# Optimization experiments

Measured on AMD Instinct MI355X. Metric: run time of the kernel, lower is better.

Reference implementation:

```python
import jax, jax.numpy as jnp
import numpy as np

B, T, D, H, V = 512, 40, 300, 200, 50257  # batch, max_length, embed_size, lstm_dimension, vocab
FORGET_BIAS = 1.0  # TF1 LSTMCell default


def setup_inputs() -> dict:
    key = jax.random.key(0)
    ks = jax.random.split(key, 8)
    s = 0.02
    return {
        "input_ids": jax.random.randint(ks[0], (B, T), 0, V, dtype=jnp.int32),
        "lengths": jax.random.randint(ks[1], (B,), 1, T + 1, dtype=jnp.int32),
        "emb": (jax.random.normal(ks[2], (V, D)) * s).astype(jnp.float32),
        "Wx": (jax.random.normal(ks[3], (D, 4 * H)) * s).astype(jnp.float32),
        "Wh": (jax.random.normal(ks[4], (H, 4 * H)) * s).astype(jnp.float32),
        "b": jnp.zeros((4 * H,), jnp.float32),
        "U": (jax.random.normal(ks[5], (H, D)) * s).astype(jnp.float32),
        "b1": jnp.zeros((D,), jnp.float32),
        "b2": jnp.zeros((V,), jnp.float32),
    }


def lstm_last_cell(x, lengths, Wx, Wh, b):
    """TF1 LSTMCell (gate order i, j, f, o; forget_bias=1) unrolled like
    dynamic_rnn with sequence_length: state frozen past each row's length.
    Returns final cell state c of shape [B, H]."""
    Bq = x.shape[0]
    Hq = Wh.shape[0]
    xt = jnp.transpose(x, (1, 0, 2))                      # [T, B, D]
    xproj = xt @ Wx + b                                    # [T, B, 4H] precomputed input GEMM
    tmask = (jnp.arange(x.shape[1])[:, None] < lengths[None, :])[..., None]  # [T, B, 1]

    def step(carry, inp):
        c, h = carry
        xp, m = inp
        gates = xp + h @ Wh                                # [B, 4H]
        i, j, f, o = jnp.split(gates, 4, axis=-1)
        c_new = jax.nn.sigmoid(f + FORGET_BIAS) * c + jax.nn.sigmoid(i) * jnp.tanh(j)
        h_new = jax.nn.sigmoid(o) * jnp.tanh(c_new)
        c = jnp.where(m, c_new, c)
        h = jnp.where(m, h_new, h)
        return (c, h), None

    init = (jnp.zeros((Bq, Hq), x.dtype), jnp.zeros((Bq, Hq), x.dtype))
    (c, _h), _ = jax.lax.scan(step, init, (xproj, tmask))
    return c


def reference(input_ids, lengths, emb, Wx, Wh, b, U, b1, b2):
    x = emb[input_ids]                                     # [B, T, D] embedding lookup
    c = lstm_last_cell(x, lengths, Wx, Wh, b)              # [B, H] final cell state (state.c)
    h1 = jax.nn.relu(c @ U + b1)                           # [B, D]
    # dropout with keep_prob=1 at eval -> identity
    return h1 @ emb.T + b2                                 # [B, V] tied-weight logits
```

## Files before the change

### kernel.cpp

```cpp
#include <hip/hip_runtime.h>
#include <stdint.h>

#define TT_  40
#define GP_  896
#define HKP_ 224
#define V_   50257
#define VP_  50432

typedef __attribute__((ext_vector_type(4))) float f32x4;
typedef __attribute__((ext_vector_type(8))) short s16x8;

__device__ __forceinline__ ushort bfrn(float f) {
  union { float f; uint32_t u; } x; x.f = f;
  return (ushort)((x.u + 0x7fffu + ((x.u >> 16) & 1u)) >> 16);
}
__device__ __forceinline__ float bl16(uint32_t u) { return __uint_as_float(u << 16); }
__device__ __forceinline__ float bh16(uint32_t u) { return __uint_as_float(u & 0xffff0000u); }
__device__ __forceinline__ float sigm(float x) { return 1.f / (1.f + __expf(-x)); }
__device__ __forceinline__ float tanh_f(float x) { return 1.f - 2.f / (__expf(2.f*x) + 1.f); }

template<int N> struct IC { static constexpr int v = N; };

__global__ void k_prep_emb(const float* __restrict__ emb, ushort* __restrict__ emb_bf) {
  const int idx = blockIdx.x * 256 + threadIdx.x;
  const int v = idx / 80, kc = idx % 80;
  ushort4 o = {0, 0, 0, 0};
  if (v < V_ && kc < 75) {
    const float4 f = *(const float4*)(emb + (size_t)v * 300 + kc * 4);
    o.x = bfrn(f.x); o.y = bfrn(f.y); o.z = bfrn(f.z); o.w = bfrn(f.w);
  }
  *(ushort4*)(emb_bf + (size_t)v * 320 + kc * 4) = o;
}

__global__ void k_prep_small(const float* __restrict__ Wx, const float* __restrict__ Wh,
                             const float* __restrict__ U, ushort* __restrict__ Wxp,
                             ushort* __restrict__ Whp, float* __restrict__ Ut) {
  int idx = blockIdx.x * 256 + threadIdx.x;
  if (idx < 896 * 320) {
    const int colp = idx / 320, k = idx % 320;
    const int n = colp >> 2, g = colp & 3;
    const float v = (colp < 800 && k < 300) ? Wx[(size_t)k * 800 + g * 200 + n] : 0.f;
    Wxp[idx] = bfrn(v);
    return;
  }
  idx -= 896 * 320;
  if (idx < 896 * 224) {
    const int colp = idx / 224, k = idx % 224;
    const int n = colp >> 2, g = colp & 3;
    const float v = (colp < 800 && k < 200) ? Wh[(size_t)k * 800 + g * 200 + n] : 0.f;
    Whp[idx] = bfrn(v);
    return;
  }
  idx -= 896 * 224;
  if (idx < 300 * 200) {
    const int d = idx / 200, h = idx % 200;
    Ut[idx] = U[(size_t)h * 300 + d];
  }
}

__global__ __launch_bounds__(256) void k_xproj(
    const int* __restrict__ ids, const ushort* __restrict__ emb_bf,
    const ushort* __restrict__ Wxp, const float* __restrict__ bias,
    ushort* __restrict__ xp) {
  __shared__ ushort bsm[70 * 512];
  const int tid = threadIdx.x;
  const int w = tid >> 6, lane = tid & 63;
  const int l15 = lane & 15, q = lane >> 4;
  const int wgm = blockIdx.x, wgn = blockIdx.y;
  const int t = wgm >> 3;
  const int bbase = (wgm & 7) << 6;
  const int n0 = wgn * 112;

  for (int s = w; s < 70; s += 4) {
    const int tl = s / 10, kb = s % 10;
    const s16x8 v = *(const s16x8*)(Wxp + (size_t)(n0 + tl * 16 + l15) * 320 + kb * 32 + q * 8);
    *(s16x8*)(&bsm[s * 512 + lane * 8]) = v;
  }
  const int brow = bbase + w * 16 + l15;
  const int id = ids[brow * TT_ + t];
  const ushort* arow = emb_bf + (size_t)id * 320;
  __syncthreads();

  f32x4 acc[7];
  const f32x4 z = {0.f, 0.f, 0.f, 0.f};
#pragma unroll
  for (int tl = 0; tl < 7; ++tl) acc[tl] = z;
  for (int kb = 0; kb < 10; ++kb) {
    const s16x8 af = *(const s16x8*)(arow + kb * 32 + q * 8);
#pragma unroll
    for (int tl = 0; tl < 7; ++tl) {
      const s16x8 bfv = *(const s16x8*)(&bsm[(tl * 10 + kb) * 512 + lane * 8]);
      acc[tl] = __builtin_amdgcn_mfma_f32_16x16x32_bf16(af, bfv, acc[tl], 0, 0, 0);
    }
  }
  const int rowbase = t * 512 + bbase + w * 16 + q * 4;
#pragma unroll
  for (int tl = 0; tl < 7; ++tl) {
    const int colp = n0 + tl * 16 + l15;
    const float bv = (colp < 800) ? bias[(colp & 3) * 200 + (colp >> 2)] : 0.f;
#pragma unroll
    for (int r = 0; r < 4; ++r)
      xp[(size_t)(rowbase + r) * GP_ + colp] = bfrn(acc[tl][r] + bv);
  }
}

__global__ __launch_bounds__(512) __attribute__((amdgpu_waves_per_eu(2, 2)))
void k_lstm(
    const ushort* __restrict__ xp, const ushort* __restrict__ Whp,
    const int* __restrict__ lengths, const float* __restrict__ Ut,
    const float* __restrict__ b1v, ushort* __restrict__ h1bf) {
  __shared__ ushort h_lds[2][3584];
  __shared__ ushort wh56_lds[57344];
  __shared__ float  c_lds[16 * 228];

  const int tid = threadIdx.x;
  const int w = tid >> 6, lane = tid & 63;
  const int l15 = lane & 15, q = lane >> 4;
  const int b0 = blockIdx.x << 4;
  const int len = lengths[b0 + l15];

  s16x8 whf[7][5];
#pragma unroll
  for (int tl = 0; tl < 7; ++tl) {
    const ushort* wr = Whp + (size_t)((w * 7 + tl) * 16 + l15) * HKP_;
#pragma unroll
    for (int kb = 0; kb < 5; ++kb)
      whf[tl][kb] = *(const s16x8*)(wr + kb * 32 + q * 8);
    *(s16x8*)(&wh56_lds[(w * 7 + tl) * 1024 + lane * 8])       = *(const s16x8*)(wr + 160 + q * 8);
    *(s16x8*)(&wh56_lds[(w * 7 + tl) * 1024 + 512 + lane * 8]) = *(const s16x8*)(wr + 192 + q * 8);
  }
  for (int i = tid; i < 3584; i += 512) ((uint32_t*)h_lds)[i] = 0;
  for (int i = tid; i < 16 * 228; i += 512) c_lds[i] = 0.f;

  int hwoff[7];
  unsigned nokm = 0;
#pragma unroll
  for (int tl = 0; tl < 7; ++tl) {
    const int T0 = w * 7 + tl;
    const int n = T0 * 4 + q;
    if (n < 200) nokm |= (1u << tl);
    hwoff[tl] = (n >> 5) * 1024 + (l15 + (((n >> 3) & 3) << 4)) * 16 + (n & 7) * 2;
  }
  const int cidx = l15 * 228 + w * 28 + q;
  const char* xbase = (const char*)xp + (size_t)(b0 + l15) * (GP_ * 2) + w * 224 + q * 8;

  __syncthreads();

  auto step = [&](int t, auto BUFC) {
    constexpr int BUF = decltype(BUFC)::v;
    const char* xpp = xbase + (size_t)t * (512 * GP_ * 2);
    uint2 xv[7];
#pragma unroll
    for (int tl = 0; tl < 7; ++tl) xv[tl] = *(const uint2*)(xpp + tl * 32);

    f32x4 acc[7];
    const f32x4 z = {0.f, 0.f, 0.f, 0.f};
#pragma unroll
    for (int tl = 0; tl < 7; ++tl) acc[tl] = z;
#pragma unroll
    for (int kb = 0; kb < 7; ++kb) {
      const s16x8 hh = *(const s16x8*)(&h_lds[BUF][kb * 512 + lane * 8]);
#pragma unroll
      for (int tl = 0; tl < 7; ++tl) {
        s16x8 a;
        if (kb < 5) a = whf[tl][kb];
        else        a = *(const s16x8*)(&wh56_lds[(w * 7 + tl) * 1024 + (kb - 5) * 512 + lane * 8]);
        acc[tl] = __builtin_amdgcn_mfma_f32_16x16x32_bf16(a, hh, acc[tl], 0, 0, 0);
      }
    }
    const bool act = (t < len);
#pragma unroll
    for (int tl = 0; tl < 7; ++tl) {
      const float g0 = acc[tl][0] + bl16(xv[tl].x);
      const float g1 = acc[tl][1] + bh16(xv[tl].x);
      const float g2 = acc[tl][2] + bl16(xv[tl].y);
      const float g3 = acc[tl][3] + bh16(xv[tl].y);
      const bool nok = (nokm >> tl) & 1;
      ushort hv = *(const ushort*)((const char*)(&h_lds[BUF][0]) + hwoff[tl]);
      if (act && nok) {
        const float cold = c_lds[cidx + 4 * tl];
        const float sf = sigm(g2 + 1.f);
        const float si = sigm(g0);
        const float tj = tanh_f(g1);
        const float cn = sf * cold + si * tj;
        c_lds[cidx + 4 * tl] = cn;
        hv = bfrn(sigm(g3) * tanh_f(cn));
      }
      if (nok)
        *(ushort*)((char*)(&h_lds[BUF ^ 1][0]) + hwoff[tl]) = hv;
    }
    __syncthreads();
  };

  for (int tt = 0; tt < TT_ / 2; ++tt) {
    step(2 * tt,     IC<0>{});
    step(2 * tt + 1, IC<1>{});
  }

  for (int i = tid; i < 4800; i += 512) {
    const int col = i >> 4, row = i & 15;
    const float* ut = Ut + col * 200;
    const float* cr = &c_lds[row * 228];
    float s = 0.f;
    for (int k = 0; k < 200; k += 4) {
      const float4 cc = *(const float4*)(cr + k);
      const float4 uu = *(const float4*)(ut + k);
      s += cc.x * uu.x + cc.y * uu.y + cc.z * uu.z + cc.w * uu.w;
    }
    s += b1v[col];
    h1bf[(size_t)(b0 + row) * 320 + col] = bfrn(fmaxf(s, 0.f));
  }
  if (tid < 320) {
    const int row = tid & 15, col = 300 + (tid >> 4);
    h1bf[(size_t)(b0 + row) * 320 + col] = 0;
  }
}

__global__ __launch_bounds__(256) void k_out(
    const ushort* __restrict__ h1bf, const ushort* __restrict__ emb_bf,
    const float* __restrict__ b2, float* __restrict__ out) {
  const int tid = threadIdx.x;
  const int w = tid >> 6, lane = tid & 63;
  const int l15 = lane & 15, q = lane >> 4;
  const int m0 = blockIdx.y << 6;
  const int n0 = blockIdx.x * 256 + w * 64;
  f32x4 acc[4][4];
  const f32x4 z = {0.f, 0.f, 0.f, 0.f};
#pragma unroll
  for (int a = 0; a < 4; ++a)
#pragma unroll
    for (int b = 0; b < 4; ++b) acc[a][b] = z;
  for (int kb = 0; kb < 10; ++kb) {
    s16x8 af[4], bfv[4];
#pragma unroll
    for (int mt = 0; mt < 4; ++mt)
      af[mt] = *(const s16x8*)(h1bf + (size_t)(m0 + mt * 16 + l15) * 320 + kb * 32 + q * 8);
#pragma unroll
    for (int nt = 0; nt < 4; ++nt)
      bfv[nt] = *(const s16x8*)(emb_bf + (size_t)(n0 + nt * 16 + l15) * 320 + kb * 32 + q * 8);
#pragma unroll
    for (int mt = 0; mt < 4; ++mt)
#pragma unroll
      for (int nt = 0; nt < 4; ++nt)
        acc[mt][nt] = __builtin_amdgcn_mfma_f32_16x16x32_bf16(af[mt], bfv[nt], acc[mt][nt], 0, 0, 0);
  }
#pragma unroll
  for (int nt = 0; nt < 4; ++nt) {
    const int col = n0 + nt * 16 + l15;
    if (col < V_) {
      const float bb = b2[col];
#pragma unroll
      for (int mt = 0; mt < 4; ++mt) {
        const int row = m0 + mt * 16 + q * 4;
#pragma unroll
        for (int r = 0; r < 4; ++r)
          out[(size_t)(row + r) * V_ + col] = acc[mt][nt][r] + bb;
      }
    }
  }
}

extern "C" void kernel_launch(void* const* d_in, const int* in_sizes, int n_in,
                              void* d_out, int out_size, void* d_ws, size_t ws_size,
                              hipStream_t stream) {
  (void)in_sizes; (void)n_in; (void)out_size; (void)ws_size;
  const int*   ids  = (const int*)d_in[0];
  const int*   lens = (const int*)d_in[1];
  const float* emb  = (const float*)d_in[2];
  const float* Wx   = (const float*)d_in[3];
  const float* Wh   = (const float*)d_in[4];
  const float* bg   = (const float*)d_in[5];
  const float* U    = (const float*)d_in[6];
  const float* b1   = (const float*)d_in[7];
  const float* b2   = (const float*)d_in[8];
  float* out = (float*)d_out;

  char* ws = (char*)d_ws;
  ushort* emb_bf = (ushort*)(ws);
  ushort* Wxp    = (ushort*)(ws + 32276480);
  ushort* Whp    = (ushort*)(ws + 32849920);
  float*  Ut     = (float*)(ws + 33251328);
  ushort* h1bf   = (ushort*)(ws + 33491328);
  ushort* xp     = (ushort*)((char*)d_out + 66226176);

  k_prep_emb  <<<15760, 256, 0, stream>>>(emb, emb_bf);
  k_prep_small<<<2139,  256, 0, stream>>>(Wx, Wh, U, Wxp, Whp, Ut);
  k_xproj     <<<dim3(320, 8), 256, 0, stream>>>(ids, emb_bf, Wxp, bg, xp);
  k_lstm      <<<32, 512, 0, stream>>>(xp, Whp, lens, Ut, b1, h1bf);
  k_out       <<<dim3(197, 8), 256, 0, stream>>>(h1bf, emb_bf, b2, out);
}
```

Before: 388.4 us.

## Spread LSTM recurrence over 14 waves and store xproj in MFMA fragment order

The LSTM block grows from 8 to 16 waves, with 14 active ones each owning 4 gate tiles instead of 7. This shortens the serial per-step MFMA chain and the gate math on the critical path. The xproj kernel now writes its output in a tiled layout that matches each wave's fragment, so the per-step loads in the recurrence are contiguous and coalesced. The cost is more waves per CU contending at each step's barrier, and the waves_per_eu hint is dropped, which may change register allocation.

```diff
diff --git a/kernel.cpp b/kernel.cpp
--- a/kernel.cpp
+++ b/kernel.cpp
@@ -2,7 +2,6 @@
 #include <stdint.h>
 
 #define TT_  40
-#define GP_  896
 #define HKP_ 224
 #define V_   50257
 #define VP_  50432
@@ -93,18 +92,21 @@
       acc[tl] = __builtin_amdgcn_mfma_f32_16x16x32_bf16(af, bfv, acc[tl], 0, 0, 0);
     }
   }
-  const int rowbase = t * 512 + bbase + w * 16 + q * 4;
+  const int g16 = ((wgm & 7) << 2) + w;
+  ushort* xpb = xp + ((size_t)t * 32 + g16) * 14336;
 #pragma unroll
   for (int tl = 0; tl < 7; ++tl) {
     const int colp = n0 + tl * 16 + l15;
+    const int T0 = colp >> 4;
     const float bv = (colp < 800) ? bias[(colp & 3) * 200 + (colp >> 2)] : 0.f;
+    const int base = T0 * 256 + (l15 >> 2) * 64 + (l15 & 3);
 #pragma unroll
     for (int r = 0; r < 4; ++r)
-      xp[(size_t)(rowbase + r) * GP_ + colp] = bfrn(acc[tl][r] + bv);
-  }
-}
-
-__global__ __launch_bounds__(512) __attribute__((amdgpu_waves_per_eu(2, 2)))
+      xpb[base + (q * 4 + r) * 4] = bfrn(acc[tl][r] + bv);
+  }
+}
+
+__global__ __launch_bounds__(1024)
 void k_lstm(
     const ushort* __restrict__ xp, const ushort* __restrict__ Whp,
     const int* __restrict__ lengths, const float* __restrict__ Ut,
@@ -116,78 +118,84 @@
   const int tid = threadIdx.x;
   const int w = tid >> 6, lane = tid & 63;
   const int l15 = lane & 15, q = lane >> 4;
-  const int b0 = blockIdx.x << 4;
+  const int g16 = blockIdx.x;
+  const int b0 = g16 << 4;
   const int len = lengths[b0 + l15];
-
-  s16x8 whf[7][5];
-#pragma unroll
-  for (int tl = 0; tl < 7; ++tl) {
-    const ushort* wr = Whp + (size_t)((w * 7 + tl) * 16 + l15) * HKP_;
-#pragma unroll
-    for (int kb = 0; kb < 5; ++kb)
-      whf[tl][kb] = *(const s16x8*)(wr + kb * 32 + q * 8);
-    *(s16x8*)(&wh56_lds[(w * 7 + tl) * 1024 + lane * 8])       = *(const s16x8*)(wr + 160 + q * 8);
-    *(s16x8*)(&wh56_lds[(w * 7 + tl) * 1024 + 512 + lane * 8]) = *(const s16x8*)(wr + 192 + q * 8);
-  }
-  for (int i = tid; i < 3584; i += 512) ((uint32_t*)h_lds)[i] = 0;
-  for (int i = tid; i < 16 * 228; i += 512) c_lds[i] = 0.f;
-
-  int hwoff[7];
+  const bool work = (w < 14);
+
+  s16x8 whf[4][5];
+  if (work) {
+#pragma unroll
+    for (int tl = 0; tl < 4; ++tl) {
+      const int T0 = w * 4 + tl;
+      const ushort* wr = Whp + (size_t)(T0 * 16 + l15) * HKP_;
+#pragma unroll
+      for (int kb = 0; kb < 5; ++kb)
+        whf[tl][kb] = *(const s16x8*)(wr + kb * 32 + q * 8);
+      *(s16x8*)(&wh56_lds[T0 * 1024 + lane * 8])       = *(const s16x8*)(wr + 160 + q * 8);
+      *(s16x8*)(&wh56_lds[T0 * 1024 + 512 + lane * 8]) = *(const s16x8*)(wr + 192 + q * 8);
+    }
+  }
+  for (int i = tid; i < 3584; i += 1024) ((uint32_t*)h_lds)[i] = 0;
+  for (int i = tid; i < 16 * 228; i += 1024) c_lds[i] = 0.f;
+
   unsigned nokm = 0;
 #pragma unroll
-  for (int tl = 0; tl < 7; ++tl) {
-    const int T0 = w * 7 + tl;
-    const int n = T0 * 4 + q;
+  for (int tl = 0; tl < 4; ++tl) {
+    const int n = (w * 4 + tl) * 4 + q;
     if (n < 200) nokm |= (1u << tl);
-    hwoff[tl] = (n >> 5) * 1024 + (l15 + (((n >> 3) & 3) << 4)) * 16 + (n & 7) * 2;
-  }
-  const int cidx = l15 * 228 + w * 28 + q;
-  const char* xbase = (const char*)xp + (size_t)(b0 + l15) * (GP_ * 2) + w * 224 + q * 8;
+  }
+  const int cidx = l15 * 228 + w * 16 + q;
+  const char* xbase = (const char*)xp + ((size_t)g16 * 28672 + (w * 4) * 512 + lane * 8);
 
   __syncthreads();
 
   auto step = [&](int t, auto BUFC) {
     constexpr int BUF = decltype(BUFC)::v;
-    const char* xpp = xbase + (size_t)t * (512 * GP_ * 2);
-    uint2 xv[7];
-#pragma unroll
-    for (int tl = 0; tl < 7; ++tl) xv[tl] = *(const uint2*)(xpp + tl * 32);
-
-    f32x4 acc[7];
-    const f32x4 z = {0.f, 0.f, 0.f, 0.f};
-#pragma unroll
-    for (int tl = 0; tl < 7; ++tl) acc[tl] = z;
-#pragma unroll
-    for (int kb = 0; kb < 7; ++kb) {
-      const s16x8 hh = *(const s16x8*)(&h_lds[BUF][kb * 512 + lane * 8]);
-#pragma unroll
-      for (int tl = 0; tl < 7; ++tl) {
-        s16x8 a;
-        if (kb < 5) a = whf[tl][kb];
-        else        a = *(const s16x8*)(&wh56_lds[(w * 7 + tl) * 1024 + (kb - 5) * 512 + lane * 8]);
-        acc[tl] = __builtin_amdgcn_mfma_f32_16x16x32_bf16(a, hh, acc[tl], 0, 0, 0);
+    if (work) {
+      const char* xpp = xbase + (size_t)t * (32 * 28672);
+      uint2 xv[4];
+#pragma unroll
+      for (int tl = 0; tl < 4; ++tl) xv[tl] = *(const uint2*)(xpp + tl * 512);
+
+      f32x4 acc[4];
+      const f32x4 z = {0.f, 0.f, 0.f, 0.f};
+#pragma unroll
+      for (int tl = 0; tl < 4; ++tl) acc[tl] = z;
+#pragma unroll
+      for (int kb = 0; kb < 7; ++kb) {
+        const s16x8 hh = *(const s16x8*)(&h_lds[BUF][kb * 512 + lane * 8]);
+#pragma unroll
+        for (int tl = 0; tl < 4; ++tl) {
+          s16x8 a;
+          if (kb < 5) a = whf[tl][kb];
+          else        a = *(const s16x8*)(&wh56_lds[(w * 4 + tl) * 1024 + (kb - 5) * 512 + lane * 8]);
+          acc[tl] = __builtin_amdgcn_mfma_f32_16x16x32_bf16(a, hh, acc[tl], 0, 0, 0);
+        }
       }
-    }
-    const bool act = (t < len);
-#pragma unroll
-    for (int tl = 0; tl < 7; ++tl) {
-      const float g0 = acc[tl][0] + bl16(xv[tl].x);
-      const float g1 = acc[tl][1] + bh16(xv[tl].x);
-      const float g2 = acc[tl][2] + bl16(xv[tl].y);
-      const float g3 = acc[tl][3] + bh16(xv[tl].y);
-      const bool nok = (nokm >> tl) & 1;
-      ushort hv = *(const ushort*)((const char*)(&h_lds[BUF][0]) + hwoff[tl]);
-      if (act && nok) {
-        const float cold = c_lds[cidx + 4 * tl];
-        const float sf = sigm(g2 + 1.f);
-        const float si = sigm(g0);
-        const float tj = tanh_f(g1);
-        const float cn = sf * cold + si * tj;
-        c_lds[cidx + 4 * tl] = cn;
-        hv = bfrn(sigm(g3) * tanh_f(cn));
+      const bool act = (t < len);
+#pragma unroll
+      for (int tl = 0; tl < 4; ++tl) {
+        const float g0 = acc[tl][0] + bl16(xv[tl].x);
+        const float g1 = acc[tl][1] + bh16(xv[tl].x);
+        const float g2 = acc[tl][2] + bl16(xv[tl].y);
+        const float g3 = acc[tl][3] + bh16(xv[tl].y);
+        const int n = (w * 4 + tl) * 4 + q;
+        const int hwoff = (n >> 5) * 1024 + (l15 + (((n >> 3) & 3) << 4)) * 16 + (n & 7) * 2;
+        const bool nok = (nokm >> tl) & 1;
+        ushort hv = *(const ushort*)((const char*)(&h_lds[BUF][0]) + hwoff);
+        if (act && nok) {
+          const float cold = c_lds[cidx + 4 * tl];
+          const float sf = sigm(g2 + 1.f);
+          const float si = sigm(g0);
+          const float tj = tanh_f(g1);
+          const float cn = sf * cold + si * tj;
+          c_lds[cidx + 4 * tl] = cn;
+          hv = bfrn(sigm(g3) * tanh_f(cn));
+        }
+        if (nok)
+          *(ushort*)((char*)(&h_lds[BUF ^ 1][0]) + hwoff) = hv;
       }
-      if (nok)
-        *(ushort*)((char*)(&h_lds[BUF ^ 1][0]) + hwoff[tl]) = hv;
     }
     __syncthreads();
   };
@@ -197,7 +205,7 @@
     step(2 * tt + 1, IC<1>{});
   }
 
-  for (int i = tid; i < 4800; i += 512) {
+  for (int i = tid; i < 4800; i += 1024) {
     const int col = i >> 4, row = i & 15;
     const float* ut = Ut + col * 200;
     const float* cr = &c_lds[row * 228];
@@ -286,6 +294,6 @@
   k_prep_emb  <<<15760, 256, 0, stream>>>(emb, emb_bf);
   k_prep_small<<<2139,  256, 0, stream>>>(Wx, Wh, U, Wxp, Whp, Ut);
   k_xproj     <<<dim3(320, 8), 256, 0, stream>>>(ids, emb_bf, Wxp, bg, xp);
-  k_lstm      <<<32, 512, 0, stream>>>(xp, Whp, lens, Ut, b1, h1bf);
+  k_lstm      <<<32, 1024, 0, stream>>>(xp, Whp, lens, Ut, b1, h1bf);
   k_out       <<<dim3(197, 8), 256, 0, stream>>>(h1bf, emb_bf, b2, out);
 }
```

Result: no change. 389.3 us (+0.2%).
